# Optimization experiments

Measured on AMD Instinct MI355X. Metric: run time of the kernel, lower is better.

The kernel has to match this reference:

```python
import jax, jax.numpy as jnp
import numpy as np

N_NODES = 50000
N_EDGES = 600000
D = 128
H_MLP = 256
N_LABELS = 10
EPS = 0.0  # tf_geometric GIN default eps


def _gin_layer(x, src, dst, W, b):
    # gather neighbor (source) features and sum-aggregate into destinations
    msg = x[src]                                   # [E, D] irregular gather
    agg = jax.ops.segment_sum(msg, dst, num_segments=N_NODES)  # [N, D]
    h = (1.0 + EPS) * x + agg                      # GIN sum update
    return jax.nn.relu(h @ W + b)                  # dense transform + relu


def setup_inputs() -> dict:
    key = jax.random.key(0)
    ks = jax.random.split(key, 8)
    x = jax.random.normal(ks[0], (N_NODES, D), dtype=jnp.float32)
    edge_index = jax.random.randint(ks[1], (2, N_EDGES), 0, N_NODES, dtype=jnp.int32)
    s = 1.0 / np.sqrt(D)
    W0 = jax.random.normal(ks[2], (D, D), dtype=jnp.float32) * s
    W1 = jax.random.normal(ks[3], (D, D), dtype=jnp.float32) * s
    W2 = jax.random.normal(ks[4], (D, D), dtype=jnp.float32) * s
    Wm1 = jax.random.normal(ks[5], (D, H_MLP), dtype=jnp.float32) * s
    Wm2 = jax.random.normal(ks[6], (H_MLP, N_LABELS), dtype=jnp.float32) * (1.0 / np.sqrt(H_MLP))
    return {
        'x': x, 'edge_index': edge_index,
        'W0': W0, 'b0': jnp.zeros((D,), jnp.float32),
        'W1': W1, 'b1': jnp.zeros((D,), jnp.float32),
        'W2': W2, 'b2': jnp.zeros((D,), jnp.float32),
        'Wm1': Wm1, 'bm1': jnp.zeros((H_MLP,), jnp.float32),
        'Wm2': Wm2, 'bm2': jnp.zeros((N_LABELS,), jnp.float32),
    }


def reference(x, edge_index, W0, b0, W1, b1, W2, b2, Wm1, bm1, Wm2, bm2):
    src, dst = edge_index[0], edge_index[1]
    h = _gin_layer(x, src, dst, W0, b0)
    h = _gin_layer(h, src, dst, W1, b1)
    h = _gin_layer(h, src, dst, W2, b2)
    # head: Flatten is identity on [N, D]; Dense(256, relu) -> Dense(num_labels)
    h = jax.nn.relu(h @ Wm1 + bm1)
    return h @ Wm2 + bm2  # [N, num_labels] logits
```

## Files before the change

### kernel.cpp

```cpp
#include <hip/hip_runtime.h>


typedef short short8 __attribute__((ext_vector_type(8)));
typedef float v4f __attribute__((ext_vector_type(4)));

#define BCAP 1024
#define MAXB 1024

__device__ inline unsigned short f2bf(float f) {
  union { float f; unsigned int u; } c; c.f = f;
  unsigned int u = c.u;
  return (unsigned short)((u + 0x7fffu + ((u >> 16) & 1u)) >> 16);
}
__device__ inline float bfbits2f(unsigned int hi) {
  union { unsigned int u; float f; } c; c.u = hi; return c.f;
}
__device__ inline unsigned int pack2(float a, float b) {
  return (unsigned int)f2bf(a) | ((unsigned int)f2bf(b) << 16);
}
__device__ inline void add8(float* s, uint4 v) {
  s[0] += bfbits2f(v.x << 16); s[1] += bfbits2f(v.x & 0xffff0000u);
  s[2] += bfbits2f(v.y << 16); s[3] += bfbits2f(v.y & 0xffff0000u);
  s[4] += bfbits2f(v.z << 16); s[5] += bfbits2f(v.z & 0xffff0000u);
  s[6] += bfbits2f(v.w << 16); s[7] += bfbits2f(v.w & 0xffff0000u);
}
__device__ inline int wave_incl_scan_int(int v, int lane) {
#pragma unroll
  for (int off = 1; off < 64; off <<= 1) {
    int t = __shfl_up(v, off, 64);
    if (lane >= off) v += t;
  }
  return v;
}

__global__ __launch_bounds__(256) void prep_all(
    const float* __restrict__ W0, const float* __restrict__ W1, const float* __restrict__ W2,
    const float* __restrict__ Wm1, const float* __restrict__ Wm2,
    unsigned short* __restrict__ W0T, unsigned short* __restrict__ W1T,
    unsigned short* __restrict__ W2T, unsigned short* __restrict__ Wm1T,
    unsigned short* __restrict__ Wm2T,
    const float* __restrict__ x, unsigned short* __restrict__ xb, int n8,
    int* __restrict__ bcnt) {
  int i = blockIdx.x * 256 + threadIdx.x;
  if (i < MAXB) bcnt[i] = 0;
  if (i < n8) {
    const float4* p = (const float4*)x;
    float4 a = p[2 * (size_t)i], b = p[2 * (size_t)i + 1];
    uint4 o;
    o.x = pack2(a.x, a.y); o.y = pack2(a.z, a.w);
    o.z = pack2(b.x, b.y); o.w = pack2(b.z, b.w);
    ((uint4*)xb)[i] = o;
  }
  if (i < 49152) {
    int w = i / 16384, r = i % 16384;
    int nn = r >> 7, k = r & 127;
    const float* W = (w == 0) ? W0 : (w == 1) ? W1 : W2;
    unsigned short* O = (w == 0) ? W0T : (w == 1) ? W1T : W2T;
    O[r] = f2bf(W[k * 128 + nn]);
  } else if (i < 49152 + 32768) {
    int r = i - 49152;
    int nn = r >> 7, k = r & 127;
    Wm1T[r] = f2bf(Wm1[k * 256 + nn]);
  } else if (i < 49152 + 32768 + 4096) {
    int r = i - 49152 - 32768;
    int nn = r >> 8, k = r & 255;
    Wm2T[r] = (nn < 10) ? f2bf(Wm2[k * 10 + nn]) : (unsigned short)0;
  }
}

__global__ __launch_bounds__(256) void bin_edges(
    const int* __restrict__ src, const int* __restrict__ dst, int E, int per,
    int* __restrict__ bcnt, int* __restrict__ bucketA, int nbuckets) {
  __shared__ int hist[MAXB];
  __shared__ int base[MAXB];
  const int tid = threadIdx.x;
  const int e0 = blockIdx.x * per;
  const int e1 = (e0 + per < E) ? e0 + per : E;
  for (int j = tid; j < nbuckets; j += 256) hist[j] = 0;
  __syncthreads();
  for (int i = e0 + tid; i < e1; i += 256) atomicAdd(&hist[dst[i] >> 6], 1);
  __syncthreads();
  for (int j = tid; j < nbuckets; j += 256) {
    int h = hist[j];
    base[j] = h ? atomicAdd(&bcnt[j], h) : 0;
  }
  __syncthreads();
  for (int i = e0 + tid; i < e1; i += 256) {
    int d = dst[i], s = src[i];
    int b = d >> 6;
    int r = atomicAdd(&base[b], 1);
    bucketA[(size_t)b * BCAP + r] = (s << 6) | (d & 63);
  }
}

__global__ __launch_bounds__(256) void sort_buckets(
    const int* __restrict__ bcnt, const int* __restrict__ bucketA,
    int* __restrict__ srcsS, int* __restrict__ boffs) {
  __shared__ int rawE[BCAP];
  __shared__ int hist[64], cur[64], offs[65];
  const int tid = threadIdx.x;
  const int b = blockIdx.x;
  const int cnt = bcnt[b];
  for (int i = tid; i < cnt; i += 256) rawE[i] = bucketA[(size_t)b * BCAP + i];
  if (tid < 64) hist[tid] = 0;
  __syncthreads();
  for (int i = tid; i < cnt; i += 256) atomicAdd(&hist[rawE[i] & 63], 1);
  __syncthreads();
  if (tid < 64) {
    int v = hist[tid];
    int incl = wave_incl_scan_int(v, tid);
    offs[tid] = incl - v;
    cur[tid] = incl - v;
    if (tid == 63) offs[64] = incl;
  }
  __syncthreads();
  for (int i = tid; i < cnt; i += 256) {
    int e = rawE[i];
    int p = atomicAdd(&cur[e & 63], 1);
    srcsS[(size_t)b * BCAP + p] = e >> 6;
  }
  if (tid < 65) boffs[b * 65 + tid] = offs[tid];
}

__global__ __launch_bounds__(256) void fused_layer(
    const unsigned short* __restrict__ X, const int* __restrict__ bcnt,
    const int* __restrict__ srcsS, const int* __restrict__ boffs,
    const unsigned short* __restrict__ BT, const float* __restrict__ bias,
    unsigned short* __restrict__ C, int M) {
  __shared__ __align__(16) unsigned short As[64 * 136];
  __shared__ int srcS[BCAP];
  __shared__ int offs[65];
  const int tid = threadIdx.x;
  const int lane = tid & 63;
  const int b = blockIdx.x;
  const int blk = b * 64;
  const int cnt = bcnt[b];

  if (tid < 65) offs[tid] = boffs[b * 65 + tid];
  for (int i = tid; i < cnt; i += 256) srcS[i] = srcsS[(size_t)b * BCAP + i];
  __syncthreads();

  const int l = tid & 15, g = tid >> 4;
  const uint4* base = (const uint4*)X;
#pragma unroll
  for (int s2 = 0; s2 < 4; ++s2) {
    int nl = s2 * 16 + g;
    int node = blk + nl;
    float s[8] = {0, 0, 0, 0, 0, 0, 0, 0};
    if (node < M) {
      add8(s, base[(size_t)node * 16 + l]);
      int beg = offs[nl], c = offs[nl + 1] - beg;
      int j = 0;
      for (; j + 8 <= c; j += 8) {
        int i0 = srcS[beg + j + 0], i1 = srcS[beg + j + 1];
        int i2 = srcS[beg + j + 2], i3 = srcS[beg + j + 3];
        int i4 = srcS[beg + j + 4], i5 = srcS[beg + j + 5];
        int i6 = srcS[beg + j + 6], i7 = srcS[beg + j + 7];
        uint4 v0 = base[(size_t)i0 * 16 + l];
        uint4 v1 = base[(size_t)i1 * 16 + l];
        uint4 v2 = base[(size_t)i2 * 16 + l];
        uint4 v3 = base[(size_t)i3 * 16 + l];
        uint4 v4 = base[(size_t)i4 * 16 + l];
        uint4 v5 = base[(size_t)i5 * 16 + l];
        uint4 v6 = base[(size_t)i6 * 16 + l];
        uint4 v7 = base[(size_t)i7 * 16 + l];
        add8(s, v0); add8(s, v1); add8(s, v2); add8(s, v3);
        add8(s, v4); add8(s, v5); add8(s, v6); add8(s, v7);
      }
      if (j + 4 <= c) {
        int i0 = srcS[beg + j + 0], i1 = srcS[beg + j + 1];
        int i2 = srcS[beg + j + 2], i3 = srcS[beg + j + 3];
        uint4 v0 = base[(size_t)i0 * 16 + l];
        uint4 v1 = base[(size_t)i1 * 16 + l];
        uint4 v2 = base[(size_t)i2 * 16 + l];
        uint4 v3 = base[(size_t)i3 * 16 + l];
        add8(s, v0); add8(s, v1); add8(s, v2); add8(s, v3);
        j += 4;
      }
      if (j + 2 <= c) {
        int i0 = srcS[beg + j + 0], i1 = srcS[beg + j + 1];
        uint4 v0 = base[(size_t)i0 * 16 + l];
        uint4 v1 = base[(size_t)i1 * 16 + l];
        add8(s, v0); add8(s, v1);
        j += 2;
      }
      if (j < c) add8(s, base[(size_t)srcS[beg + j] * 16 + l]);
    }
    uint4 o;
    o.x = pack2(s[0], s[1]); o.y = pack2(s[2], s[3]);
    o.z = pack2(s[4], s[5]); o.w = pack2(s[6], s[7]);
    *(uint4*)&As[nl * 136 + l * 8] = o;
  }
  __syncthreads();

  const int w = tid >> 6;
  const int wm = w & 1, wn = w >> 1;
  const int l15 = lane & 15, quad = lane >> 4;
  const int mb = wm * 32, nb2 = wn * 64;

  const unsigned short* bp[4];
#pragma unroll
  for (int nf = 0; nf < 4; ++nf)
    bp[nf] = BT + (size_t)(nb2 + nf * 16 + l15) * 128 + quad * 8;

  v4f acc[2][4];
#pragma unroll
  for (int mf = 0; mf < 2; ++mf)
#pragma unroll
    for (int nf = 0; nf < 4; ++nf) acc[mf][nf] = (v4f)0.f;

#pragma unroll
  for (int k0 = 0; k0 < 128; k0 += 32) {
    short8 a[2], bv[4];
#pragma unroll
    for (int mf = 0; mf < 2; ++mf)
      a[mf] = *(const short8*)&As[(mb + mf * 16 + l15) * 136 + k0 + quad * 8];
#pragma unroll
    for (int nf = 0; nf < 4; ++nf) bv[nf] = *(const short8*)(bp[nf] + k0);
#pragma unroll
    for (int mf = 0; mf < 2; ++mf)
#pragma unroll
      for (int nf = 0; nf < 4; ++nf)
        acc[mf][nf] = __builtin_amdgcn_mfma_f32_16x16x32_bf16(a[mf], bv[nf], acc[mf][nf], 0, 0, 0);
  }

#pragma unroll
  for (int mf = 0; mf < 2; ++mf) {
#pragma unroll
    for (int r = 0; r < 4; ++r) {
      int grow = blk + mb + mf * 16 + quad * 4 + r;
      if (grow >= M) continue;
#pragma unroll
      for (int nf = 0; nf < 4; ++nf) {
        int gcol = nb2 + nf * 16 + l15;
        float v = acc[mf][nf][r] + bias[gcol];
        C[(size_t)grow * 128 + gcol] = f2bf(fmaxf(v, 0.f));
      }
    }
  }
}

__global__ __launch_bounds__(256) void fused_l3_head(
    const unsigned short* __restrict__ X, const int* __restrict__ bcnt,
    const int* __restrict__ srcsS, const int* __restrict__ boffs,
    const unsigned short* __restrict__ W2T, const float* __restrict__ b2,
    const unsigned short* __restrict__ Wm1T, const float* __restrict__ bm1,
    const unsigned short* __restrict__ Wm2T, const float* __restrict__ bm2,
    float* __restrict__ out, int M, int NOUT) {
  __shared__ __align__(16) unsigned char lds[64 * 264 * 2];
  unsigned short* As = (unsigned short*)lds;
  int* srcS = (int*)(lds + 64 * 136 * 2);
  unsigned short* Hs = (unsigned short*)lds;
  __shared__ int offs[65];
  const int tid = threadIdx.x;
  const int lane = tid & 63;
  const int b = blockIdx.x;
  const int blk = b * 64;
  const int cnt = bcnt[b];

  if (tid < 65) offs[tid] = boffs[b * 65 + tid];
  for (int i = tid; i < cnt; i += 256) srcS[i] = srcsS[(size_t)b * BCAP + i];
  __syncthreads();

  const int l = tid & 15, g = tid >> 4;
  const uint4* base = (const uint4*)X;
#pragma unroll
  for (int s2 = 0; s2 < 4; ++s2) {
    int nl = s2 * 16 + g;
    int node = blk + nl;
    float s[8] = {0, 0, 0, 0, 0, 0, 0, 0};
    if (node < M) {
      add8(s, base[(size_t)node * 16 + l]);
      int beg = offs[nl], c = offs[nl + 1] - beg;
      int j = 0;
      for (; j + 8 <= c; j += 8) {
        int i0 = srcS[beg + j + 0], i1 = srcS[beg + j + 1];
        int i2 = srcS[beg + j + 2], i3 = srcS[beg + j + 3];
        int i4 = srcS[beg + j + 4], i5 = srcS[beg + j + 5];
        int i6 = srcS[beg + j + 6], i7 = srcS[beg + j + 7];
        uint4 v0 = base[(size_t)i0 * 16 + l];
        uint4 v1 = base[(size_t)i1 * 16 + l];
        uint4 v2 = base[(size_t)i2 * 16 + l];
        uint4 v3 = base[(size_t)i3 * 16 + l];
        uint4 v4 = base[(size_t)i4 * 16 + l];
        uint4 v5 = base[(size_t)i5 * 16 + l];
        uint4 v6 = base[(size_t)i6 * 16 + l];
        uint4 v7 = base[(size_t)i7 * 16 + l];
        add8(s, v0); add8(s, v1); add8(s, v2); add8(s, v3);
        add8(s, v4); add8(s, v5); add8(s, v6); add8(s, v7);
      }
      if (j + 4 <= c) {
        int i0 = srcS[beg + j + 0], i1 = srcS[beg + j + 1];
        int i2 = srcS[beg + j + 2], i3 = srcS[beg + j + 3];
        uint4 v0 = base[(size_t)i0 * 16 + l];
        uint4 v1 = base[(size_t)i1 * 16 + l];
        uint4 v2 = base[(size_t)i2 * 16 + l];
        uint4 v3 = base[(size_t)i3 * 16 + l];
        add8(s, v0); add8(s, v1); add8(s, v2); add8(s, v3);
        j += 4;
      }
      if (j + 2 <= c) {
        int i0 = srcS[beg + j + 0], i1 = srcS[beg + j + 1];
        uint4 v0 = base[(size_t)i0 * 16 + l];
        uint4 v1 = base[(size_t)i1 * 16 + l];
        add8(s, v0); add8(s, v1);
        j += 2;
      }
      if (j < c) add8(s, base[(size_t)srcS[beg + j] * 16 + l]);
    }
    uint4 o;
    o.x = pack2(s[0], s[1]); o.y = pack2(s[2], s[3]);
    o.z = pack2(s[4], s[5]); o.w = pack2(s[6], s[7]);
    *(uint4*)&As[nl * 136 + l * 8] = o;
  }
  __syncthreads();

  const int w = tid >> 6;
  const int wm = w & 1, wn = w >> 1;
  const int l15 = lane & 15, quad = lane >> 4;
  const int mb = wm * 32, nb2 = wn * 64;

  v4f acc[2][4];
#pragma unroll
  for (int mf = 0; mf < 2; ++mf)
#pragma unroll
    for (int nf = 0; nf < 4; ++nf) acc[mf][nf] = (v4f)0.f;

#pragma unroll
  for (int k0 = 0; k0 < 128; k0 += 32) {
    short8 a[2], bv[4];
#pragma unroll
    for (int mf = 0; mf < 2; ++mf)
      a[mf] = *(const short8*)&As[(mb + mf * 16 + l15) * 136 + k0 + quad * 8];
#pragma unroll
    for (int nf = 0; nf < 4; ++nf)
      bv[nf] = *(const short8*)(W2T + (size_t)(nb2 + nf * 16 + l15) * 128 + quad * 8 + k0);
#pragma unroll
    for (int mf = 0; mf < 2; ++mf)
#pragma unroll
      for (int nf = 0; nf < 4; ++nf)
        acc[mf][nf] = __builtin_amdgcn_mfma_f32_16x16x32_bf16(a[mf], bv[nf], acc[mf][nf], 0, 0, 0);
  }
  __syncthreads();

#pragma unroll
  for (int mf = 0; mf < 2; ++mf)
#pragma unroll
    for (int r = 0; r < 4; ++r) {
      int row = mb + mf * 16 + quad * 4 + r;
#pragma unroll
      for (int nf = 0; nf < 4; ++nf) {
        int col = nb2 + nf * 16 + l15;
        As[row * 136 + col] = f2bf(fmaxf(acc[mf][nf][r] + b2[col], 0.f));
      }
    }
  __syncthreads();

  const int nbH = wn * 128;
  v4f acc2[2][8];
#pragma unroll
  for (int mf = 0; mf < 2; ++mf)
#pragma unroll
    for (int nf = 0; nf < 8; ++nf) acc2[mf][nf] = (v4f)0.f;

#pragma unroll
  for (int k0 = 0; k0 < 128; k0 += 32) {
    short8 a[2];
#pragma unroll
    for (int mf = 0; mf < 2; ++mf)
      a[mf] = *(const short8*)&As[(mb + mf * 16 + l15) * 136 + k0 + quad * 8];
#pragma unroll
    for (int nf = 0; nf < 8; ++nf) {
      short8 bb = *(const short8*)(Wm1T + (size_t)(nbH + nf * 16 + l15) * 128 + quad * 8 + k0);
#pragma unroll
      for (int mf = 0; mf < 2; ++mf)
        acc2[mf][nf] = __builtin_amdgcn_mfma_f32_16x16x32_bf16(a[mf], bb, acc2[mf][nf], 0, 0, 0);
    }
  }
  __syncthreads();

#pragma unroll
  for (int mf = 0; mf < 2; ++mf)
#pragma unroll
    for (int r = 0; r < 4; ++r) {
      int row = mb + mf * 16 + quad * 4 + r;
#pragma unroll
      for (int nf = 0; nf < 8; ++nf) {
        int col = nbH + nf * 16 + l15;
        Hs[row * 264 + col] = f2bf(fmaxf(acc2[mf][nf][r] + bm1[col], 0.f));
      }
    }
  __syncthreads();

  const int rowl = w * 16 + l15;
  const unsigned short* bp2 = Wm2T + (size_t)l15 * 256 + quad * 8;
  v4f acc3 = (v4f)0.f;
#pragma unroll
  for (int k0 = 0; k0 < 256; k0 += 32)
    acc3 = __builtin_amdgcn_mfma_f32_16x16x32_bf16(
        *(const short8*)&Hs[rowl * 264 + k0 + quad * 8],
        *(const short8*)(bp2 + k0), acc3, 0, 0, 0);
  float bb = (l15 < NOUT) ? bm2[l15] : 0.f;
#pragma unroll
  for (int r = 0; r < 4; ++r) {
    int grow = blk + w * 16 + quad * 4 + r;
    if (grow < M && l15 < NOUT) out[(size_t)grow * NOUT + l15] = acc3[r] + bb;
  }
}


extern "C" void kernel_launch(void* const* d_in, const int* in_sizes, int n_in,
                              void* d_out, int out_size, void* d_ws, size_t ws_size,
                              hipStream_t stream) {
  const float* x   = (const float*)d_in[0];
  const int*   ei  = (const int*)d_in[1];
  const float* W0  = (const float*)d_in[2];
  const float* b0  = (const float*)d_in[3];
  const float* W1  = (const float*)d_in[4];
  const float* b1  = (const float*)d_in[5];
  const float* W2  = (const float*)d_in[6];
  const float* b2  = (const float*)d_in[7];
  const float* Wm1 = (const float*)d_in[8];
  const float* bm1 = (const float*)d_in[9];
  const float* Wm2 = (const float*)d_in[10];
  const float* bm2 = (const float*)d_in[11];
  float* out = (float*)d_out;

  const int D = 128;
  const int N = in_sizes[0] / D;
  const int E = in_sizes[1] / 2;
  const int L = in_sizes[11];
  const int nb = (N + 63) / 64;

  const int* srcv = ei;
  const int* dstv = ei + E;

  char* ws = (char*)d_ws;
  size_t off = 0;
  auto alloc = [&](size_t bytes) -> void* {
    void* p = ws + off;
    off = (off + bytes + 255) & ~(size_t)255;
    return p;
  };
  int* bcnt    = (int*)alloc((size_t)MAXB * 4);
  int* bucketA = (int*)alloc((size_t)nb * BCAP * 4);
  int* srcsS   = (int*)alloc((size_t)nb * BCAP * 4);
  int* boffs   = (int*)alloc((size_t)nb * 65 * 4);
  unsigned short* xb   = (unsigned short*)alloc((size_t)N * 128 * 2);
  unsigned short* h1   = (unsigned short*)alloc((size_t)N * 128 * 2);
  unsigned short* h2   = (unsigned short*)alloc((size_t)N * 128 * 2);
  unsigned short* W0T  = (unsigned short*)alloc(128 * 128 * 2);
  unsigned short* W1T  = (unsigned short*)alloc(128 * 128 * 2);
  unsigned short* W2T  = (unsigned short*)alloc(128 * 128 * 2);
  unsigned short* Wm1T = (unsigned short*)alloc(256 * 128 * 2);
  unsigned short* Wm2T = (unsigned short*)alloc(16 * 256 * 2);
  (void)ws_size; (void)n_in; (void)out_size;

  const int tpb = 256;
  int n8 = N * 16;
  prep_all<<<dim3((n8 + tpb - 1) / tpb), dim3(tpb), 0, stream>>>(
      W0, W1, W2, Wm1, Wm2, W0T, W1T, W2T, Wm1T, Wm2T, x, xb, n8, bcnt);

  const int nbin = 128;
  int per = (E + nbin - 1) / nbin;
  bin_edges<<<dim3(nbin), dim3(tpb), 0, stream>>>(srcv, dstv, E, per, bcnt, bucketA, nb);
  sort_buckets<<<dim3(nb), dim3(tpb), 0, stream>>>(bcnt, bucketA, srcsS, boffs);

  dim3 lgrid(nb);
  fused_layer<<<lgrid, dim3(tpb), 0, stream>>>(xb, bcnt, srcsS, boffs, W0T, b0, h1, N);
  fused_layer<<<lgrid, dim3(tpb), 0, stream>>>(h1, bcnt, srcsS, boffs, W1T, b1, h2, N);
  fused_l3_head<<<lgrid, dim3(tpb), 0, stream>>>(h2, bcnt, srcsS, boffs, W2T, b2,
                                                 Wm1T, bm1, Wm2T, bm2, out, N, L);
}
```

Measured before the change: 241.1 us.

## Gather neighbors via padded 16-slot index table with zero-row sentinel

The sort stage now also writes a per-node padded neighbor table of 16 slots, filling unused slots with index N, which points at an extra all-zero feature row appended to each feature buffer. The gather in each layer loads its node's 16 indices with one coalesced read, broadcasts them with shuffles, and issues 16 independent row loads with no branches. Nodes with more than 16 neighbors fall back to a serial loop over the sorted list. This removes the per-block LDS staging of the index list and the branchy 8/4/2/1 remainder loops so more loads are in flight. In exchange every node spends 16 loads even when its degree is lower, which adds extra reads of the zero row.

```diff
diff --git a/kernel.cpp b/kernel.cpp
--- a/kernel.cpp
+++ b/kernel.cpp
@@ -40,9 +40,17 @@
     unsigned short* __restrict__ W2T, unsigned short* __restrict__ Wm1T,
     unsigned short* __restrict__ Wm2T,
     const float* __restrict__ x, unsigned short* __restrict__ xb, int n8,
-    int* __restrict__ bcnt) {
+    int* __restrict__ bcnt, unsigned short* __restrict__ h1,
+    unsigned short* __restrict__ h2, int N) {
   int i = blockIdx.x * 256 + threadIdx.x;
   if (i < MAXB) bcnt[i] = 0;
+  if (blockIdx.x == 0) {
+    int t = threadIdx.x;
+    uint4 z = make_uint4(0, 0, 0, 0);
+    if (t < 16)            ((uint4*)xb)[(size_t)N * 16 + t] = z;
+    else if (t < 32)       ((uint4*)h1)[(size_t)N * 16 + (t - 16)] = z;
+    else if (t < 48)       ((uint4*)h2)[(size_t)N * 16 + (t - 32)] = z;
+  }
   if (i < n8) {
     const float4* p = (const float4*)x;
     float4 a = p[2 * (size_t)i], b = p[2 * (size_t)i + 1];
@@ -95,11 +103,13 @@
 
 __global__ __launch_bounds__(256) void sort_buckets(
     const int* __restrict__ bcnt, const int* __restrict__ bucketA,
-    int* __restrict__ srcsS, int* __restrict__ boffs) {
-  __shared__ int rawE[BCAP];
+    int* __restrict__ srcsS, int* __restrict__ srcsPad,
+    int* __restrict__ boffs, int N) {
+  __shared__ int rawE[BCAP], sortedS[BCAP];
   __shared__ int hist[64], cur[64], offs[65];
   const int tid = threadIdx.x;
   const int b = blockIdx.x;
+  const int blk = b * 64;
   const int cnt = bcnt[b];
   for (int i = tid; i < cnt; i += 256) rawE[i] = bucketA[(size_t)b * BCAP + i];
   if (tid < 64) hist[tid] = 0;
@@ -117,83 +127,71 @@
   for (int i = tid; i < cnt; i += 256) {
     int e = rawE[i];
     int p = atomicAdd(&cur[e & 63], 1);
-    srcsS[(size_t)b * BCAP + p] = e >> 6;
+    sortedS[p] = e >> 6;
+  }
+  __syncthreads();
+  for (int i = tid; i < cnt; i += 256) srcsS[(size_t)b * BCAP + i] = sortedS[i];
+  for (int idx = tid; idx < 1024; idx += 256) {
+    int nl = idx >> 4, j = idx & 15;
+    int beg = offs[nl], c = offs[nl + 1] - beg;
+    srcsPad[((size_t)(blk + nl)) * 16 + j] = (j < c) ? sortedS[beg + j] : N;
   }
   if (tid < 65) boffs[b * 65 + tid] = offs[tid];
 }
 
+__device__ inline void gather64(const uint4* __restrict__ base,
+                                const int* __restrict__ srcsPad,
+                                const int* __restrict__ srcsS, size_t bucketBase,
+                                const int* __restrict__ offs,
+                                unsigned short* __restrict__ As,
+                                int blk, int M, int tid) {
+  const int l = tid & 15, g = tid >> 4;
+  const int gb = (tid & 63) & 48;
+#pragma unroll 1
+  for (int s2 = 0; s2 < 4; ++s2) {
+    const int nl = s2 * 16 + g;
+    const int node = blk + nl;
+    const int nrow = (node < M) ? node : M;
+    const int beg = offs[nl];
+    const int c = offs[nl + 1] - beg;
+    const int myidx = srcsPad[(size_t)node * 16 + l];
+    uint4 self = base[(size_t)nrow * 16 + l];
+    uint4 r[16];
+#pragma unroll
+    for (int j = 0; j < 16; ++j) {
+      int ij = __shfl(myidx, gb + j, 64);
+      r[j] = base[(size_t)ij * 16 + l];
+    }
+    float s[8] = {0, 0, 0, 0, 0, 0, 0, 0};
+    add8(s, self);
+#pragma unroll
+    for (int j = 0; j < 16; ++j) add8(s, r[j]);
+    for (int j = 16; j < c; ++j)
+      add8(s, base[(size_t)srcsS[bucketBase + beg + j] * 16 + l]);
+    uint4 o;
+    o.x = pack2(s[0], s[1]); o.y = pack2(s[2], s[3]);
+    o.z = pack2(s[4], s[5]); o.w = pack2(s[6], s[7]);
+    *(uint4*)&As[nl * 136 + l * 8] = o;
+  }
+}
+
 __global__ __launch_bounds__(256) void fused_layer(
-    const unsigned short* __restrict__ X, const int* __restrict__ bcnt,
+    const unsigned short* __restrict__ X, const int* __restrict__ srcsPad,
     const int* __restrict__ srcsS, const int* __restrict__ boffs,
     const unsigned short* __restrict__ BT, const float* __restrict__ bias,
     unsigned short* __restrict__ C, int M) {
   __shared__ __align__(16) unsigned short As[64 * 136];
-  __shared__ int srcS[BCAP];
   __shared__ int offs[65];
   const int tid = threadIdx.x;
-  const int lane = tid & 63;
   const int b = blockIdx.x;
   const int blk = b * 64;
-  const int cnt = bcnt[b];
-
   if (tid < 65) offs[tid] = boffs[b * 65 + tid];
-  for (int i = tid; i < cnt; i += 256) srcS[i] = srcsS[(size_t)b * BCAP + i];
-  __syncthreads();
-
-  const int l = tid & 15, g = tid >> 4;
-  const uint4* base = (const uint4*)X;
-#pragma unroll
-  for (int s2 = 0; s2 < 4; ++s2) {
-    int nl = s2 * 16 + g;
-    int node = blk + nl;
-    float s[8] = {0, 0, 0, 0, 0, 0, 0, 0};
-    if (node < M) {
-      add8(s, base[(size_t)node * 16 + l]);
-      int beg = offs[nl], c = offs[nl + 1] - beg;
-      int j = 0;
-      for (; j + 8 <= c; j += 8) {
-        int i0 = srcS[beg + j + 0], i1 = srcS[beg + j + 1];
-        int i2 = srcS[beg + j + 2], i3 = srcS[beg + j + 3];
-        int i4 = srcS[beg + j + 4], i5 = srcS[beg + j + 5];
-        int i6 = srcS[beg + j + 6], i7 = srcS[beg + j + 7];
-        uint4 v0 = base[(size_t)i0 * 16 + l];
-        uint4 v1 = base[(size_t)i1 * 16 + l];
-        uint4 v2 = base[(size_t)i2 * 16 + l];
-        uint4 v3 = base[(size_t)i3 * 16 + l];
-        uint4 v4 = base[(size_t)i4 * 16 + l];
-        uint4 v5 = base[(size_t)i5 * 16 + l];
-        uint4 v6 = base[(size_t)i6 * 16 + l];
-        uint4 v7 = base[(size_t)i7 * 16 + l];
-        add8(s, v0); add8(s, v1); add8(s, v2); add8(s, v3);
-        add8(s, v4); add8(s, v5); add8(s, v6); add8(s, v7);
-      }
-      if (j + 4 <= c) {
-        int i0 = srcS[beg + j + 0], i1 = srcS[beg + j + 1];
-        int i2 = srcS[beg + j + 2], i3 = srcS[beg + j + 3];
-        uint4 v0 = base[(size_t)i0 * 16 + l];
-        uint4 v1 = base[(size_t)i1 * 16 + l];
-        uint4 v2 = base[(size_t)i2 * 16 + l];
-        uint4 v3 = base[(size_t)i3 * 16 + l];
-        add8(s, v0); add8(s, v1); add8(s, v2); add8(s, v3);
-        j += 4;
-      }
-      if (j + 2 <= c) {
-        int i0 = srcS[beg + j + 0], i1 = srcS[beg + j + 1];
-        uint4 v0 = base[(size_t)i0 * 16 + l];
-        uint4 v1 = base[(size_t)i1 * 16 + l];
-        add8(s, v0); add8(s, v1);
-        j += 2;
-      }
-      if (j < c) add8(s, base[(size_t)srcS[beg + j] * 16 + l]);
-    }
-    uint4 o;
-    o.x = pack2(s[0], s[1]); o.y = pack2(s[2], s[3]);
-    o.z = pack2(s[4], s[5]); o.w = pack2(s[6], s[7]);
-    *(uint4*)&As[nl * 136 + l * 8] = o;
-  }
-  __syncthreads();
-
-  const int w = tid >> 6;
+  __syncthreads();
+
+  gather64((const uint4*)X, srcsPad, srcsS, (size_t)b * BCAP, offs, As, blk, M, tid);
+  __syncthreads();
+
+  const int lane = tid & 63, w = tid >> 6;
   const int wm = w & 1, wn = w >> 1;
   const int l15 = lane & 15, quad = lane >> 4;
   const int mb = wm * 32, nb2 = wn * 64;
@@ -241,7 +239,7 @@
 }
 
 __global__ __launch_bounds__(256) void fused_l3_head(
-    const unsigned short* __restrict__ X, const int* __restrict__ bcnt,
+    const unsigned short* __restrict__ X, const int* __restrict__ srcsPad,
     const int* __restrict__ srcsS, const int* __restrict__ boffs,
     const unsigned short* __restrict__ W2T, const float* __restrict__ b2,
     const unsigned short* __restrict__ Wm1T, const float* __restrict__ bm1,
@@ -249,83 +247,28 @@
     float* __restrict__ out, int M, int NOUT) {
   __shared__ __align__(16) unsigned char lds[64 * 264 * 2];
   unsigned short* As = (unsigned short*)lds;
-  int* srcS = (int*)(lds + 64 * 136 * 2);
   unsigned short* Hs = (unsigned short*)lds;
   __shared__ int offs[65];
   const int tid = threadIdx.x;
-  const int lane = tid & 63;
   const int b = blockIdx.x;
   const int blk = b * 64;
-  const int cnt = bcnt[b];
-
   if (tid < 65) offs[tid] = boffs[b * 65 + tid];
-  for (int i = tid; i < cnt; i += 256) srcS[i] = srcsS[(size_t)b * BCAP + i];
-  __syncthreads();
-
-  const int l = tid & 15, g = tid >> 4;
-  const uint4* base = (const uint4*)X;
-#pragma unroll
-  for (int s2 = 0; s2 < 4; ++s2) {
-    int nl = s2 * 16 + g;
-    int node = blk + nl;
-    float s[8] = {0, 0, 0, 0, 0, 0, 0, 0};
-    if (node < M) {
-      add8(s, base[(size_t)node * 16 + l]);
-      int beg = offs[nl], c = offs[nl + 1] - beg;
-      int j = 0;
-      for (; j + 8 <= c; j += 8) {
-        int i0 = srcS[beg + j + 0], i1 = srcS[beg + j + 1];
-        int i2 = srcS[beg + j + 2], i3 = srcS[beg + j + 3];
-        int i4 = srcS[beg + j + 4], i5 = srcS[beg + j + 5];
-        int i6 = srcS[beg + j + 6], i7 = srcS[beg + j + 7];
-        uint4 v0 = base[(size_t)i0 * 16 + l];
-        uint4 v1 = base[(size_t)i1 * 16 + l];
-        uint4 v2 = base[(size_t)i2 * 16 + l];
-        uint4 v3 = base[(size_t)i3 * 16 + l];
-        uint4 v4 = base[(size_t)i4 * 16 + l];
-        uint4 v5 = base[(size_t)i5 * 16 + l];
-        uint4 v6 = base[(size_t)i6 * 16 + l];
-        uint4 v7 = base[(size_t)i7 * 16 + l];
-        add8(s, v0); add8(s, v1); add8(s, v2); add8(s, v3);
-        add8(s, v4); add8(s, v5); add8(s, v6); add8(s, v7);
-      }
-      if (j + 4 <= c) {
-        int i0 = srcS[beg + j + 0], i1 = srcS[beg + j + 1];
-        int i2 = srcS[beg + j + 2], i3 = srcS[beg + j + 3];
-        uint4 v0 = base[(size_t)i0 * 16 + l];
-        uint4 v1 = base[(size_t)i1 * 16 + l];
-        uint4 v2 = base[(size_t)i2 * 16 + l];
-        uint4 v3 = base[(size_t)i3 * 16 + l];
-        add8(s, v0); add8(s, v1); add8(s, v2); add8(s, v3);
-        j += 4;
-      }
-      if (j + 2 <= c) {
-        int i0 = srcS[beg + j + 0], i1 = srcS[beg + j + 1];
-        uint4 v0 = base[(size_t)i0 * 16 + l];
-        uint4 v1 = base[(size_t)i1 * 16 + l];
-        add8(s, v0); add8(s, v1);
-        j += 2;
-      }
-      if (j < c) add8(s, base[(size_t)srcS[beg + j] * 16 + l]);
-    }
-    uint4 o;
-    o.x = pack2(s[0], s[1]); o.y = pack2(s[2], s[3]);
-    o.z = pack2(s[4], s[5]); o.w = pack2(s[6], s[7]);
-    *(uint4*)&As[nl * 136 + l * 8] = o;
-  }
-  __syncthreads();
-
-  const int w = tid >> 6;
+  __syncthreads();
+
+  gather64((const uint4*)X, srcsPad, srcsS, (size_t)b * BCAP, offs, As, blk, M, tid);
+  __syncthreads();
+
+  const int lane = tid & 63, w = tid >> 6;
   const int wm = w & 1, wn = w >> 1;
   const int l15 = lane & 15, quad = lane >> 4;
-  const int mb = wm * 32, nb2 = wn * 64;
-
+  const int mb = wm * 32;
+
+  const int nb2 = wn * 64;
   v4f acc[2][4];
 #pragma unroll
   for (int mf = 0; mf < 2; ++mf)
 #pragma unroll
     for (int nf = 0; nf < 4; ++nf) acc[mf][nf] = (v4f)0.f;
-
 #pragma unroll
   for (int k0 = 0; k0 < 128; k0 += 32) {
     short8 a[2], bv[4];
@@ -362,7 +305,6 @@
   for (int mf = 0; mf < 2; ++mf)
 #pragma unroll
     for (int nf = 0; nf < 8; ++nf) acc2[mf][nf] = (v4f)0.f;
-
 #pragma unroll
   for (int k0 = 0; k0 < 128; k0 += 32) {
     short8 a[2];
@@ -371,10 +313,10 @@
       a[mf] = *(const short8*)&As[(mb + mf * 16 + l15) * 136 + k0 + quad * 8];
 #pragma unroll
     for (int nf = 0; nf < 8; ++nf) {
-      short8 bb = *(const short8*)(Wm1T + (size_t)(nbH + nf * 16 + l15) * 128 + quad * 8 + k0);
+      short8 bv = *(const short8*)(Wm1T + (size_t)(nbH + nf * 16 + l15) * 128 + quad * 8 + k0);
 #pragma unroll
       for (int mf = 0; mf < 2; ++mf)
-        acc2[mf][nf] = __builtin_amdgcn_mfma_f32_16x16x32_bf16(a[mf], bb, acc2[mf][nf], 0, 0, 0);
+        acc2[mf][nf] = __builtin_amdgcn_mfma_f32_16x16x32_bf16(a[mf], bv, acc2[mf][nf], 0, 0, 0);
     }
   }
   __syncthreads();
@@ -445,10 +387,11 @@
   int* bcnt    = (int*)alloc((size_t)MAXB * 4);
   int* bucketA = (int*)alloc((size_t)nb * BCAP * 4);
   int* srcsS   = (int*)alloc((size_t)nb * BCAP * 4);
+  int* srcsPad = (int*)alloc((size_t)nb * 64 * 16 * 4);
   int* boffs   = (int*)alloc((size_t)nb * 65 * 4);
-  unsigned short* xb   = (unsigned short*)alloc((size_t)N * 128 * 2);
-  unsigned short* h1   = (unsigned short*)alloc((size_t)N * 128 * 2);
-  unsigned short* h2   = (unsigned short*)alloc((size_t)N * 128 * 2);
+  unsigned short* xb   = (unsigned short*)alloc((size_t)(N + 1) * 128 * 2);
+  unsigned short* h1   = (unsigned short*)alloc((size_t)(N + 1) * 128 * 2);
+  unsigned short* h2   = (unsigned short*)alloc((size_t)(N + 1) * 128 * 2);
   unsigned short* W0T  = (unsigned short*)alloc(128 * 128 * 2);
   unsigned short* W1T  = (unsigned short*)alloc(128 * 128 * 2);
   unsigned short* W2T  = (unsigned short*)alloc(128 * 128 * 2);
@@ -459,16 +402,16 @@
   const int tpb = 256;
   int n8 = N * 16;
   prep_all<<<dim3((n8 + tpb - 1) / tpb), dim3(tpb), 0, stream>>>(
-      W0, W1, W2, Wm1, Wm2, W0T, W1T, W2T, Wm1T, Wm2T, x, xb, n8, bcnt);
+      W0, W1, W2, Wm1, Wm2, W0T, W1T, W2T, Wm1T, Wm2T, x, xb, n8, bcnt, h1, h2, N);
 
   const int nbin = 128;
   int per = (E + nbin - 1) / nbin;
   bin_edges<<<dim3(nbin), dim3(tpb), 0, stream>>>(srcv, dstv, E, per, bcnt, bucketA, nb);
-  sort_buckets<<<dim3(nb), dim3(tpb), 0, stream>>>(bcnt, bucketA, srcsS, boffs);
+  sort_buckets<<<dim3(nb), dim3(tpb), 0, stream>>>(bcnt, bucketA, srcsS, srcsPad, boffs, N);
 
   dim3 lgrid(nb);
-  fused_layer<<<lgrid, dim3(tpb), 0, stream>>>(xb, bcnt, srcsS, boffs, W0T, b0, h1, N);
-  fused_layer<<<lgrid, dim3(tpb), 0, stream>>>(h1, bcnt, srcsS, boffs, W1T, b1, h2, N);
-  fused_l3_head<<<lgrid, dim3(tpb), 0, stream>>>(h2, bcnt, srcsS, boffs, W2T, b2,
+  fused_layer<<<lgrid, dim3(tpb), 0, stream>>>(xb, srcsPad, srcsS, boffs, W0T, b0, h1, N);
+  fused_layer<<<lgrid, dim3(tpb), 0, stream>>>(h1, srcsPad, srcsS, boffs, W1T, b1, h2, N);
+  fused_l3_head<<<lgrid, dim3(tpb), 0, stream>>>(h2, srcsPad, srcsS, boffs, W2T, b2,
                                                  Wm1T, bm1, Wm2T, bm2, out, N, L);
 }
```

Result: slower. 247.1 us (+2.5%).
